# Optimization experiments

Hardware: AMD Instinct MI355X
Metric: run time of the kernel (lower is better)

The kernel has to match this reference:

```python
import jax, jax.numpy as jnp
import numpy as np

PIXEL_W = 1.0
EPS = 1e-8
BIG = 1e10


def extract_zero_crossings(s):
    """Vectorized marching-squares-style zero-crossing extraction.
    s: (H, W) SDF. Returns padded points (N, 2) float and validity mask (N,) bool,
    N = (H-1)*W + H*(W-1), in the same (vertical pairs first, then horizontal)
    order as the original python loops."""
    H, W = s.shape
    dt = s.dtype
    # vertical neighbor pairs (i, j) vs (i+1, j)
    v1, v2 = s[:-1, :], s[1:, :]
    ii = jnp.broadcast_to(jnp.arange(H - 1, dtype=dt)[:, None], (H - 1, W))
    jj = jnp.broadcast_to(jnp.arange(W, dtype=dt)[None, :], (H - 1, W))
    c1 = v1 == 0
    c2 = (~c1) & (v2 == 0)
    cx = (~c1) & (~c2) & (v1 * v2 < 0)
    alpha = jnp.abs(v1) / (jnp.abs(v1) + jnp.abs(v2) + EPS)
    row = jnp.where(c1, ii, jnp.where(c2, ii + 1.0, ii + alpha))
    pts_v = jnp.stack([row, jj], axis=-1).reshape(-1, 2)
    m_v = (c1 | c2 | cx).reshape(-1)
    # horizontal neighbor pairs (i, j) vs (i, j+1)
    h1, h2 = s[:, :-1], s[:, 1:]
    ii2 = jnp.broadcast_to(jnp.arange(H, dtype=dt)[:, None], (H, W - 1))
    jj2 = jnp.broadcast_to(jnp.arange(W - 1, dtype=dt)[None, :], (H, W - 1))
    d1 = h1 == 0
    d2 = (~d1) & (h2 == 0)
    dx = (~d1) & (~d2) & (h1 * h2 < 0)
    beta = jnp.abs(h1) / (jnp.abs(h1) + jnp.abs(h2) + EPS)
    col = jnp.where(d1, jj2, jnp.where(d2, jj2 + 1.0, jj2 + beta))
    pts_h = jnp.stack([ii2, col], axis=-1).reshape(-1, 2)
    m_h = (d1 | d2 | dx).reshape(-1)
    return jnp.concatenate([pts_v, pts_h], 0), jnp.concatenate([m_v, m_h], 0)


def pairwise_dist(p, g):
    # (Np, Ng) euclidean distances via the gram trick (avoids (Np,Ng,2) temp)
    d2 = jnp.sum(p * p, 1)[:, None] + jnp.sum(g * g, 1)[None, :] - 2.0 * (p @ g.T)
    return jnp.sqrt(jnp.maximum(d2, 0.0))


def masked_chamfer(pp, pm, gp, gm):
    # chamfer as in compute_chamfer_distance: -mean(min over gt) + mean(min over pred)
    d = pairwise_dist(pp, gp)
    d = jnp.where(pm[:, None] & gm[None, :], d, BIG)
    min_p = jnp.min(d, axis=1)
    min_g = jnp.min(d, axis=0)
    np_ = jnp.maximum(jnp.sum(pm), 1)
    ng_ = jnp.maximum(jnp.sum(gm), 1)
    return -jnp.sum(jnp.where(pm, min_p, 0.0)) / np_ + jnp.sum(jnp.where(gm, min_g, 0.0)) / ng_


def setup_inputs() -> dict:
    key = jax.random.key(0)
    k1, k2 = jax.random.split(key)
    B, H, W = 2, 80, 80
    return {
        "pred_logits": jax.random.normal(k1, (B, 1, H, W), dtype=jnp.float32),
        "gt_sdf": jax.random.normal(k2, (B, 1, H, W), dtype=jnp.float32),
    }


def reference(pred_logits, gt_sdf):
    pred = pred_logits[:, 0]  # (B, H, W)
    gt = gt_sdf[:, 0]
    pixel_loss = jnp.mean(jnp.abs(pred - gt))
    chamfers = []
    for b in range(pred.shape[0]):  # small fixed batch loop
        pp, pm = extract_zero_crossings(pred[b])
        gp, gm = extract_zero_crossings(gt[b])
        chamfers.append(masked_chamfer(pp, pm, gp, gm))
    loss = PIXEL_W * pixel_loss
    last_chamfer = jnp.mean(jnp.stack(chamfers))
    return loss, last_chamfer
```

## Files before the change

### kernel.cpp

```cpp
#include <hip/hip_runtime.h>

#define HH 80
#define WW 80
#define IMG (HH * WW)
#define NV ((HH - 1) * WW)
#define NPTS (NV + HH * (WW - 1))
#define NPIX (2 * IMG)
#define BIGF 1.0e10f
#define INVC 1.0e7f
#define EPSF 1e-8f
#define QSCALE 131072.0f

#define PBLK 1024
#define PWAVES (PBLK / 64)
#define QTR (NPTS / PWAVES)

#define BLK 256
#define APT 4
#define ACHUNK (BLK * APT)
#define ABLOCKS ((NPTS + ACHUNK - 1) / ACHUNK)
#define NSLICE 16
#define MAXSLICE ((((NPTS + NSLICE - 1) / NSLICE) + 1) & ~1)

__device__ __forceinline__ float wave_reduce_f(float v) {
#pragma unroll
  for (int o = 32; o > 0; o >>= 1) v += __shfl_down(v, o, 64);
  return v;
}
__device__ __forceinline__ long long wave_reduce_ll(long long v) {
#pragma unroll
  for (int o = 32; o > 0; o >>= 1) {
    int2 p = *(int2*)&v;
    p.x = __shfl_down(p.x, o, 64);
    p.y = __shfl_down(p.y, o, 64);
    v += *(long long*)&p;
  }
  return v;
}

__global__ void __launch_bounds__(PBLK) k_prep(
    const float* __restrict__ pred, const float* __restrict__ gt,
    float2* __restrict__ pts, float* __restrict__ minarr,
    int* __restrict__ cnt, float* __restrict__ pixpart,
    unsigned long long* __restrict__ sum_i, unsigned int* __restrict__ ticket) {
  int set = blockIdx.x;
  int tid = threadIdx.x, lane = tid & 63, wid = tid >> 6;
  const float* s = (set < 2 ? pred : gt) + (set & 1) * IMG;

  __shared__ int wcnt_s[PWAVES];
  __shared__ float wpix_s[PWAVES];
  __shared__ int wbase_s[PWAVES];

  if (set == 0 && tid < 4) sum_i[tid] = 0ull;
  if (set == 0 && tid == 4) *ticket = 0u;

  for (int i = tid; i < NPTS; i += PBLK) minarr[set * NPTS + i] = BIGF;

  float ps = 0.f;
  for (int i = set * (NPIX / 4) + tid; i < (set + 1) * (NPIX / 4); i += PBLK)
    ps += fabsf(pred[i] - gt[i]);
  ps = wave_reduce_f(ps);
  if (lane == 0) wpix_s[wid] = ps;

  int mycnt = 0;
  int wbeg = wid * QTR;
  for (int base = 0; base < QTR; base += 64) {
    int idx = wbeg + base + lane;
    bool valid = false;
    if (base + lane < QTR) {
      if (idx < NV) {
        int i = idx / WW, j = idx - i * WW;
        float v1 = s[i * WW + j], v2 = s[(i + 1) * WW + j];
        valid = (v1 == 0.f) | (v2 == 0.f) | (v1 * v2 < 0.f);
      } else {
        int t = idx - NV;
        int i = t / (WW - 1), j = t - i * (WW - 1);
        float h1 = s[i * WW + j], h2 = s[i * WW + j + 1];
        valid = (h1 == 0.f) | (h2 == 0.f) | (h1 * h2 < 0.f);
      }
    }
    mycnt += valid ? 1 : 0;
  }
  unsigned long long m0 = __ballot(true); (void)m0;
  mycnt = (int)wave_reduce_f((float)mycnt);
  if (lane == 0) wcnt_s[wid] = mycnt;
  __syncthreads();
  if (tid == 0) {
    int b = 0;
    float px = 0.f;
    for (int w = 0; w < PWAVES; ++w) {
      wbase_s[w] = b; b += wcnt_s[w];
      px += wpix_s[w];
    }
    cnt[set] = b;
    pixpart[set] = px;
  }
  __syncthreads();

  int off = wbase_s[wid];
  for (int base = 0; base < QTR; base += 64) {
    int idx = wbeg + base + lane;
    float r = 0.f, c = 0.f;
    bool valid = false;
    if (base + lane < QTR) {
      if (idx < NV) {
        int i = idx / WW, j = idx - i * WW;
        float v1 = s[i * WW + j], v2 = s[(i + 1) * WW + j];
        c = (float)j;
        if (v1 == 0.f)      { r = (float)i;       valid = true; }
        else if (v2 == 0.f) { r = (float)i + 1.f; valid = true; }
        else {
          r = (float)i + fabsf(v1) / (fabsf(v1) + fabsf(v2) + EPSF);
          valid = (v1 * v2 < 0.f);
        }
      } else {
        int t = idx - NV;
        int i = t / (WW - 1), j = t - i * (WW - 1);
        float h1 = s[i * WW + j], h2 = s[i * WW + j + 1];
        r = (float)i;
        if (h1 == 0.f)      { c = (float)j;       valid = true; }
        else if (h2 == 0.f) { c = (float)j + 1.f; valid = true; }
        else {
          c = (float)j + fabsf(h1) / (fabsf(h1) + fabsf(h2) + EPSF);
          valid = (h1 * h2 < 0.f);
        }
      }
    }
    unsigned long long mask = __ballot(valid);
    int lpos = __popcll(mask & ((1ull << lane) - 1ull));
    if (valid) pts[set * NPTS + off + lpos] = make_float2(r, c);
    off += __popcll(mask);
  }
}

__global__ void __launch_bounds__(BLK) k_min(
    const float2* __restrict__ pts, float* __restrict__ minarr,
    const int* __restrict__ cnt) {
  int dir = blockIdx.z;
  int Aset = ((dir & 1) << 1) | (dir >> 1);
  int Bset = Aset ^ 2;
  int cntA = cnt[Aset], cntB = cnt[Bset];

  int abase0 = blockIdx.x * ACHUNK;
  if (abase0 >= cntA) return;
  int slicelen = (((cntB + NSLICE - 1) / NSLICE) + 1) & ~1;
  int b0 = blockIdx.y * slicelen;
  if (b0 >= cntB) return;
  int n = min(slicelen, cntB - b0);
  int sn = (n + 1) & ~1;

  __shared__ float4 tile[MAXSLICE];
  for (int i = threadIdx.x; i < sn; i += BLK) {
    float2 q = (i < n) ? pts[Bset * NPTS + b0 + i] : make_float2(INVC, INVC);
    tile[i] = make_float4(q.x, q.y, fmaf(q.x, q.x, q.y * q.y), 0.f);
  }
  __syncthreads();

  int abase = abase0 + threadIdx.x;
  float nx[APT], ny[APT], p2[APT], m[APT];
#pragma unroll
  for (int i = 0; i < APT; ++i) {
    int a = abase + i * BLK;
    float2 p = (a < cntA) ? pts[Aset * NPTS + a] : make_float2(0.f, 0.f);
    nx[i] = -2.f * p.x;
    ny[i] = -2.f * p.y;
    p2[i] = fmaf(p.x, p.x, p.y * p.y);
    m[i] = 3.0e38f;
  }

#pragma unroll 2
  for (int b = 0; b < sn; b += 2) {
    float4 q0 = tile[b];
    float4 q1 = tile[b + 1];
#pragma unroll
    for (int i = 0; i < APT; ++i) {
      float t0 = fmaf(ny[i], q0.y, fmaf(nx[i], q0.x, q0.z));
      float t1 = fmaf(ny[i], q1.y, fmaf(nx[i], q1.x, q1.z));
      m[i] = fminf(fminf(t0, t1), m[i]);
    }
  }

#pragma unroll
  for (int i = 0; i < APT; ++i) {
    int a = abase + i * BLK;
    if (a < cntA) {
      float d2 = fmaxf(m[i] + p2[i], 0.f);
      atomicMin((unsigned int*)&minarr[Aset * NPTS + a], __float_as_uint(d2));
    }
  }
}

__global__ void __launch_bounds__(256) k_fin(
    const float* __restrict__ minarr, const int* __restrict__ cnt,
    const float* __restrict__ pixpart, unsigned long long* __restrict__ sum_i,
    unsigned int* __restrict__ ticket, float* __restrict__ out) {
  int set = blockIdx.x >> 2, q = blockIdx.x & 3;
  int tid = threadIdx.x, lane = tid & 63;
  int n = cnt[set];

  long long ls = 0;
  for (int i = q * 256 + tid; i < n; i += 1024) {
    float d = sqrtf(minarr[set * NPTS + i]);
    ls += (long long)(d * QSCALE + 0.5f);
  }
  ls = wave_reduce_ll(ls);
  if (lane == 0) atomicAdd(&sum_i[set], (unsigned long long)ls);
  __syncthreads();

  if (tid == 0) {
    __threadfence();
    unsigned int t = atomicAdd(ticket, 1u);
    if (t == 15u) {
      float ss[4];
      for (int k = 0; k < 4; ++k)
        ss[k] = (float)((long long)atomicAdd(&sum_i[k], 0ull)) * (1.0f / QSCALE);
      float n0 = fmaxf((float)cnt[0], 1.f), n1 = fmaxf((float)cnt[1], 1.f);
      float n2 = fmaxf((float)cnt[2], 1.f), n3 = fmaxf((float)cnt[3], 1.f);
      float ch0 = -ss[0] / n0 + ss[2] / n2;
      float ch1 = -ss[1] / n1 + ss[3] / n3;
      out[0] = (pixpart[0] + pixpart[1] + pixpart[2] + pixpart[3]) / (float)NPIX;
      out[1] = 0.5f * (ch0 + ch1);
    }
  }
}

extern "C" void kernel_launch(void* const* d_in, const int* in_sizes, int n_in,
                              void* d_out, int out_size, void* d_ws, size_t ws_size,
                              hipStream_t stream) {
  const float* pred = (const float*)d_in[0];
  const float* gt   = (const float*)d_in[1];
  float* out = (float*)d_out;

  int*   cnt     = (int*)d_ws;
  float* pixpart = (float*)d_ws + 4;
  unsigned long long* sum_i = (unsigned long long*)((char*)d_ws + 32);
  unsigned int* ticket = (unsigned int*)((char*)d_ws + 64);
  float2* pts    = (float2*)((char*)d_ws + 256);
  float* minarr  = (float*)((char*)d_ws + 256 + sizeof(float2) * 4 * NPTS);

  k_prep<<<4, PBLK, 0, stream>>>(pred, gt, pts, minarr, cnt, pixpart, sum_i, ticket);
  k_min<<<dim3(ABLOCKS, NSLICE, 4), BLK, 0, stream>>>(pts, minarr, cnt);
  k_fin<<<16, 256, 0, stream>>>(minarr, cnt, pixpart, sum_i, ticket, out);
}
```

Before: 40.50 us.

## Parallelize zero-crossing extraction across many blocks with atomic compaction

```diff
diff --git a/kernel.cpp b/kernel.cpp
--- a/kernel.cpp
+++ b/kernel.cpp
@@ -11,10 +11,7 @@
 #define EPSF 1e-8f
 #define QSCALE 131072.0f
 
-#define PBLK 1024
-#define PWAVES (PBLK / 64)
-#define QTR (NPTS / PWAVES)
-
+#define NB 256
 #define BLK 256
 #define APT 4
 #define ACHUNK (BLK * APT)
@@ -22,11 +19,10 @@
 #define NSLICE 16
 #define MAXSLICE ((((NPTS + NSLICE - 1) / NSLICE) + 1) & ~1)
 
-__device__ __forceinline__ float wave_reduce_f(float v) {
-#pragma unroll
-  for (int o = 32; o > 0; o >>= 1) v += __shfl_down(v, o, 64);
-  return v;
-}
+#define SETPAD 12672
+#define EXWAVES (4 * (SETPAD / 64))
+#define PXWAVES (NPIX / 64)
+
 __device__ __forceinline__ long long wave_reduce_ll(long long v) {
 #pragma unroll
   for (int o = 32; o > 0; o >>= 1) {
@@ -38,71 +34,23 @@
   return v;
 }
 
-__global__ void __launch_bounds__(PBLK) k_prep(
+__global__ void __launch_bounds__(256) k_prep(
     const float* __restrict__ pred, const float* __restrict__ gt,
     float2* __restrict__ pts, float* __restrict__ minarr,
-    int* __restrict__ cnt, float* __restrict__ pixpart,
-    unsigned long long* __restrict__ sum_i, unsigned int* __restrict__ ticket) {
-  int set = blockIdx.x;
+    int* __restrict__ cnt, unsigned long long* __restrict__ pix_i) {
   int tid = threadIdx.x, lane = tid & 63, wid = tid >> 6;
-  const float* s = (set < 2 ? pred : gt) + (set & 1) * IMG;
-
-  __shared__ int wcnt_s[PWAVES];
-  __shared__ float wpix_s[PWAVES];
-  __shared__ int wbase_s[PWAVES];
-
-  if (set == 0 && tid < 4) sum_i[tid] = 0ull;
-  if (set == 0 && tid == 4) *ticket = 0u;
-
-  for (int i = tid; i < NPTS; i += PBLK) minarr[set * NPTS + i] = BIGF;
-
-  float ps = 0.f;
-  for (int i = set * (NPIX / 4) + tid; i < (set + 1) * (NPIX / 4); i += PBLK)
-    ps += fabsf(pred[i] - gt[i]);
-  ps = wave_reduce_f(ps);
-  if (lane == 0) wpix_s[wid] = ps;
-
-  int mycnt = 0;
-  int wbeg = wid * QTR;
-  for (int base = 0; base < QTR; base += 64) {
-    int idx = wbeg + base + lane;
-    bool valid = false;
-    if (base + lane < QTR) {
-      if (idx < NV) {
-        int i = idx / WW, j = idx - i * WW;
-        float v1 = s[i * WW + j], v2 = s[(i + 1) * WW + j];
-        valid = (v1 == 0.f) | (v2 == 0.f) | (v1 * v2 < 0.f);
-      } else {
-        int t = idx - NV;
-        int i = t / (WW - 1), j = t - i * (WW - 1);
-        float h1 = s[i * WW + j], h2 = s[i * WW + j + 1];
-        valid = (h1 == 0.f) | (h2 == 0.f) | (h1 * h2 < 0.f);
-      }
-    }
-    mycnt += valid ? 1 : 0;
-  }
-  unsigned long long m0 = __ballot(true); (void)m0;
-  mycnt = (int)wave_reduce_f((float)mycnt);
-  if (lane == 0) wcnt_s[wid] = mycnt;
-  __syncthreads();
-  if (tid == 0) {
-    int b = 0;
-    float px = 0.f;
-    for (int w = 0; w < PWAVES; ++w) {
-      wbase_s[w] = b; b += wcnt_s[w];
-      px += wpix_s[w];
-    }
-    cnt[set] = b;
-    pixpart[set] = px;
-  }
-  __syncthreads();
-
-  int off = wbase_s[wid];
-  for (int base = 0; base < QTR; base += 64) {
-    int idx = wbeg + base + lane;
+  int gtid = blockIdx.x * 256 + tid;
+
+  if (gtid < 4 * NPTS) minarr[gtid] = BIGF;
+
+  int gw = blockIdx.x * 4 + wid;
+  if (gw < EXWAVES) {
+    int set = gw / (SETPAD / 64);
+    int idx = (gw - set * (SETPAD / 64)) * 64 + lane;
+    const float* s = (set < 2 ? pred : gt) + (set & 1) * IMG;
     float r = 0.f, c = 0.f;
     bool valid = false;
-    if (base + lane < QTR) {
+    if (idx < NPTS) {
       if (idx < NV) {
         int i = idx / WW, j = idx - i * WW;
         float v1 = s[i * WW + j], v2 = s[(i + 1) * WW + j];
@@ -127,9 +75,20 @@
       }
     }
     unsigned long long mask = __ballot(valid);
-    int lpos = __popcll(mask & ((1ull << lane) - 1ull));
-    if (valid) pts[set * NPTS + off + lpos] = make_float2(r, c);
-    off += __popcll(mask);
+    int nw = __popcll(mask);
+    int base = 0;
+    if (lane == 0 && nw) base = atomicAdd(&cnt[set], nw);
+    base = __shfl(base, 0, 64);
+    if (valid) {
+      int lpos = __popcll(mask & ((1ull << lane) - 1ull));
+      pts[set * NPTS + base + lpos] = make_float2(r, c);
+    }
+  } else if (gw < EXWAVES + PXWAVES) {
+    int p = (gw - EXWAVES) * 64 + lane;
+    float d = fabsf(pred[p] - gt[p]);
+    long long q = (long long)(d * QSCALE + 0.5f);
+    q = wave_reduce_ll(q);
+    if (lane == 0) atomicAdd(pix_i, (unsigned long long)q);
   }
 }
 
@@ -192,7 +151,8 @@
 
 __global__ void __launch_bounds__(256) k_fin(
     const float* __restrict__ minarr, const int* __restrict__ cnt,
-    const float* __restrict__ pixpart, unsigned long long* __restrict__ sum_i,
+    const unsigned long long* __restrict__ pix_i,
+    unsigned long long* __restrict__ sum_i,
     unsigned int* __restrict__ ticket, float* __restrict__ out) {
   int set = blockIdx.x >> 2, q = blockIdx.x & 3;
   int tid = threadIdx.x, lane = tid & 63;
@@ -211,14 +171,15 @@
     __threadfence();
     unsigned int t = atomicAdd(ticket, 1u);
     if (t == 15u) {
+      const float iq = 1.0f / QSCALE;
       float ss[4];
       for (int k = 0; k < 4; ++k)
-        ss[k] = (float)((long long)atomicAdd(&sum_i[k], 0ull)) * (1.0f / QSCALE);
+        ss[k] = (float)((long long)atomicAdd(&sum_i[k], 0ull)) * iq;
       float n0 = fmaxf((float)cnt[0], 1.f), n1 = fmaxf((float)cnt[1], 1.f);
       float n2 = fmaxf((float)cnt[2], 1.f), n3 = fmaxf((float)cnt[3], 1.f);
       float ch0 = -ss[0] / n0 + ss[2] / n2;
       float ch1 = -ss[1] / n1 + ss[3] / n3;
-      out[0] = (pixpart[0] + pixpart[1] + pixpart[2] + pixpart[3]) / (float)NPIX;
+      out[0] = (float)(long long)(*pix_i) * iq / (float)NPIX;
       out[1] = 0.5f * (ch0 + ch1);
     }
   }
@@ -231,14 +192,15 @@
   const float* gt   = (const float*)d_in[1];
   float* out = (float*)d_out;
 
-  int*   cnt     = (int*)d_ws;
-  float* pixpart = (float*)d_ws + 4;
+  int* cnt = (int*)d_ws;
+  unsigned int* ticket = (unsigned int*)((char*)d_ws + 16);
+  unsigned long long* pix_i = (unsigned long long*)((char*)d_ws + 24);
   unsigned long long* sum_i = (unsigned long long*)((char*)d_ws + 32);
-  unsigned int* ticket = (unsigned int*)((char*)d_ws + 64);
-  float2* pts    = (float2*)((char*)d_ws + 256);
-  float* minarr  = (float*)((char*)d_ws + 256 + sizeof(float2) * 4 * NPTS);
-
-  k_prep<<<4, PBLK, 0, stream>>>(pred, gt, pts, minarr, cnt, pixpart, sum_i, ticket);
+  float2* pts   = (float2*)((char*)d_ws + 256);
+  float* minarr = (float*)((char*)d_ws + 256 + sizeof(float2) * 4 * NPTS);
+
+  hipMemsetAsync(d_ws, 0, 256, stream);
+  k_prep<<<NB, 256, 0, stream>>>(pred, gt, pts, minarr, cnt, pix_i);
   k_min<<<dim3(ABLOCKS, NSLICE, 4), BLK, 0, stream>>>(pts, minarr, cnt);
-  k_fin<<<16, 256, 0, stream>>>(minarr, cnt, pixpart, sum_i, ticket, out);
-}
+  k_fin<<<16, 256, 0, stream>>>(minarr, cnt, pix_i, sum_i, ticket, out);
+}
```

New measurement: 48.80 us. +20.5%, slower.
